# Kernel tuning notes

Hardware: AMD Instinct MI355X
Metric: run time of the kernel (lower is better)

Reference implementation:

```python
import jax, jax.numpy as jnp
import numpy as np
import math

B, S, E, H = 2, 2048, 512, 8
D = E // H
EPS = 1e-6
MAXN = 1.0 - 1e-5  # stay strictly inside the Poincare ball


def _norm(x):
    return jnp.sqrt(jnp.clip(jnp.sum(x * x, axis=-1, keepdims=True), 1e-12))


def expmap0(u):
    n = _norm(u)
    return jnp.tanh(n) * u / n


def logmap0(x):
    n = _norm(x)
    return jnp.arctanh(jnp.clip(n, None, MAXN)) * x / n


def hlinear(x, W, b):
    # HLinear: Mobius matvec == expmap0(W @ logmap0(x)), tangent bias
    return expmap0(logmap0(x) @ W.T + b)


def _lbeta(a, b):
    return math.lgamma(a) + math.lgamma(b) - math.lgamma(a + b)


def setup_inputs() -> dict:
    key = jax.random.key(0)
    ks = jax.random.split(key, 6)

    def pt(k, shape):  # random points on the Poincare ball
        return expmap0(0.2 * jax.random.normal(k, shape, dtype=jnp.float32))

    return {
        "query": pt(ks[0], (B, S, E)),
        "key": pt(ks[1], (B, S, E)),
        "value": pt(ks[2], (B, S, E)),
        "Wq": jax.random.normal(ks[3], (E, E), jnp.float32) / math.sqrt(E),
        "Wk": jax.random.normal(ks[4], (E, E), jnp.float32) / math.sqrt(E),
        "Wv": jax.random.normal(ks[5], (E, E), jnp.float32) / math.sqrt(E),
        "bq": jnp.zeros((E,), jnp.float32),
        "bk": jnp.zeros((E,), jnp.float32),
        "bv": jnp.zeros((E,), jnp.float32),
        "scale_tau": jnp.zeros((1,), jnp.float32),
        "scale_gamma": jnp.zeros((1,), jnp.float32),
    }


def reference(query, key, value, Wq, Wk, Wv, bq, bk, bv, scale_tau, scale_gamma):
    # hyperbolic q/k/v projections, then split heads: [B,H,S,D]
    q = hlinear(query, Wq, bq).reshape(B, S, H, D).transpose(0, 2, 1, 3)
    k = hlinear(key, Wk, bk).reshape(B, S, H, D).transpose(0, 2, 1, 3)
    v = hlinear(value, Wv, bv).reshape(B, S, H, D).transpose(0, 2, 1, 3)

    # pairwise Poincare distance via norms + dot (no [S,S,D] intermediate)
    qn2 = jnp.sum(q * q, -1)                       # [B,H,S]
    kn2 = jnp.sum(k * k, -1)                       # [B,H,S]
    dot = jnp.einsum('bhid,bhjd->bhij', q, k)      # [B,H,S,S]
    sq = jnp.clip(qn2[..., :, None] + kn2[..., None, :] - 2.0 * dot, 0.0)
    denom = jnp.clip((1.0 - qn2)[..., :, None] * (1.0 - kn2)[..., None, :], EPS)
    dist = jnp.arccosh(jnp.clip(1.0 + 2.0 * sq / denom, 1.0 + 1e-7))

    # attention_similarity: -d / tau + gamma, tau = 1/exp(scale_tau)
    sim = -dist * jnp.exp(scale_tau[0]) + scale_gamma[0]

    # causal mask + 'exp' activation (masked_fill(-inf) then exp -> 0)
    mask = jnp.triu(jnp.ones((S, S), bool), 1)
    w = jnp.where(mask, 0.0, jnp.exp(sim))         # [B,H,S,S]

    # gyromidpoint: (1/2) (x) [sum_j w lam_j v_j / sum_j w (lam_j - 1)]
    vn2 = jnp.sum(v * v, -1)
    lam = 2.0 / jnp.clip(1.0 - vn2, EPS)           # [B,H,S]
    num = jnp.einsum('bhij,bhjd->bhid', w, v * lam[..., None])
    den = jnp.einsum('bhij,bhj->bhi', w, lam - 1.0)
    m = num / jnp.clip(den, EPS)[..., None]
    mn = _norm(m)
    mid = jnp.tanh(0.5 * jnp.arctanh(jnp.clip(mn, None, MAXN))) * m / mn

    # beta-concatenation of heads back to embed_dim
    beta_ratio = math.exp(_lbeta(E / 2.0, 0.5) - _lbeta(D / 2.0, 0.5))
    t = logmap0(mid) * beta_ratio                  # [B,H,S,D]
    t = t.transpose(0, 2, 1, 3).reshape(B, S, E)
    return expmap0(t)
```

## Files before the change

### kernel.cpp

```cpp
#include <hip/hip_runtime.h>
#include <cmath>

#define BB 2
#define SS 2048
#define EE 512
#define HH 8
#define DD 64

typedef unsigned short u16t;
typedef __bf16 bf16x8 __attribute__((ext_vector_type(8)));
typedef float f32x4 __attribute__((ext_vector_type(4)));

__device__ __forceinline__ float bf2f(u16t u){
    union{unsigned int i; float f;} c; c.i = ((unsigned int)u)<<16; return c.f;
}
__device__ __forceinline__ u16t f2bf(float x){
    union{float f; unsigned int i;} c; c.f = x;
    return (u16t)((c.i + 0x7fffu + ((c.i>>16)&1u))>>16);
}
__device__ __forceinline__ unsigned cvtpk(float a, float b){
    unsigned r;
    asm("v_cvt_pk_bf16_f32 %0, %1, %2" : "=v"(r) : "v"(a), "v"(b));
    return r;
}
__device__ __forceinline__ float fast_tanh(float x){
    float e = __expf(2.f*x); return 1.f - 2.f/(e+1.f);
}
__device__ __forceinline__ float fast_atanh(float x){
    return 0.5f*__logf((1.f+x)/(1.f-x));
}
__device__ __forceinline__ f32x4 mfma16(bf16x8 a, bf16x8 b, f32x4 c){
    return __builtin_amdgcn_mfma_f32_16x16x32_bf16(a,b,c,0,0,0);
}
__device__ __forceinline__ int offq8(int qi){
    int a = qi >> 3;
    return 4*a*(a+1) + (qi & 7)*(a+1);
}

__global__ __launch_bounds__(256) void k_pre(const float* __restrict__ qp,
                                             const float* __restrict__ kp,
                                             const float* __restrict__ vp,
                                             u16t* __restrict__ Tlog,
                                             const float* __restrict__ Wq,
                                             const float* __restrict__ Wk,
                                             const float* __restrict__ Wv,
                                             u16t* __restrict__ Wb){
    int bx = blockIdx.x;
    if (bx < 3072){
        int gr = bx*4 + (threadIdx.x>>6);
        int t = gr >> 12;
        int row = gr & 4095;
        int lane = threadIdx.x & 63;
        const float* src = (t==0 ? qp : (t==1 ? kp : vp)) + (size_t)row*EE;
        const float4* s4 = (const float4*)(src + lane*8);
        float4 a = s4[0], b = s4[1];
        float x[8] = {a.x,a.y,a.z,a.w,b.x,b.y,b.z,b.w};
        float p = 0.f;
        #pragma unroll
        for (int i=0;i<8;++i) p += x[i]*x[i];
        #pragma unroll
        for (int off=32; off>=1; off>>=1) p += __shfl_xor(p, off, 64);
        float n = sqrtf(fmaxf(p, 1e-12f));
        float f = fast_atanh(fminf(n, 1.0f-1e-5f)) / n;
        u16t yb[8];
        #pragma unroll
        for (int i=0;i<8;++i) yb[i] = f2bf(f*x[i]);
        uint4 o;
        o.x = (unsigned)yb[0] | ((unsigned)yb[1]<<16);
        o.y = (unsigned)yb[2] | ((unsigned)yb[3]<<16);
        o.z = (unsigned)yb[4] | ((unsigned)yb[5]<<16);
        o.w = (unsigned)yb[6] | ((unsigned)yb[7]<<16);
        *(uint4*)(Tlog + ((size_t)(t*4096+row)*EE + lane*8)) = o;
    } else {
        int idx = ((bx-3072)*256 + threadIdx.x)*4;
        int t = idx >> 18;
        int off = idx & 262143;
        const float* W = (t==0 ? Wq : (t==1 ? Wk : Wv));
        float4 a = *(const float4*)(W + off);
        uint2 o;
        o.x = (unsigned)f2bf(a.x) | ((unsigned)f2bf(a.y)<<16);
        o.y = (unsigned)f2bf(a.z) | ((unsigned)f2bf(a.w)<<16);
        *(uint2*)(Wb + idx) = o;
    }
}

__global__ __launch_bounds__(256) void k_proj(const u16t* __restrict__ Tlog,
                                              const u16t* __restrict__ Wb,
                                              const float* __restrict__ bq,
                                              const float* __restrict__ bk,
                                              const float* __restrict__ bv,
                                              u16t* __restrict__ U){
    __shared__ __align__(16) u16t Wl[64][72];
    int bx = blockIdx.x;
    int t = bx >> 9; int rem = bx & 511;
    int m0 = (rem >> 3) << 6; int n0 = (rem & 7) << 6;
    int tid = threadIdx.x; int wv = tid>>6; int lane = tid&63;
    int l15 = lane & 15; int l4 = lane >> 4;
    const u16t* Tt = Tlog + (size_t)t*4096*EE;
    const u16t* Wt = Wb + (size_t)t*EE*EE;
    const float* bias = (t==0 ? bq : (t==1 ? bk : bv));
    f32x4 z = {0.f,0.f,0.f,0.f};
    f32x4 acc[4] = {z,z,z,z};
    int arow = m0 + 16*wv + l15;
    int rr = tid >> 2; int cc = (tid & 3) * 16;
    uint4 w0, w1;
    {
        const uint4* g = (const uint4*)(Wt + (size_t)(n0+rr)*EE + cc);
        w0 = g[0]; w1 = g[1];
    }
    for (int ks=0; ks<8; ++ks){
        int k0 = ks*64;
        *(uint4*)&Wl[rr][cc]   = w0;
        *(uint4*)&Wl[rr][cc+8] = w1;
        __syncthreads();
        if (ks < 7){
            const uint4* g = (const uint4*)(Wt + (size_t)(n0+rr)*EE + k0 + 64 + cc);
            w0 = g[0]; w1 = g[1];
        }
        bf16x8 a0 = *(const bf16x8*)(Tt + (size_t)arow*EE + k0 + l4*8);
        bf16x8 a1 = *(const bf16x8*)(Tt + (size_t)arow*EE + k0 + 32 + l4*8);
        #pragma unroll
        for (int f=0; f<4; ++f){
            bf16x8 b0 = *(const bf16x8*)&Wl[f*16+l15][l4*8];
            bf16x8 b1 = *(const bf16x8*)&Wl[f*16+l15][32+l4*8];
            acc[f] = mfma16(b0, a0, acc[f]);
            acc[f] = mfma16(b1, a1, acc[f]);
        }
        __syncthreads();
    }
    u16t* Ut = U + (size_t)t*4096*EE;
    int mrow = m0 + 16*wv + l15;
    #pragma unroll
    for (int f=0; f<4; ++f){
        float4 b4 = *(const float4*)&bias[n0 + f*16 + l4*4];
        uint2 u2;
        u2.x = cvtpk(acc[f][0]+b4.x, acc[f][1]+b4.y);
        u2.y = cvtpk(acc[f][2]+b4.z, acc[f][3]+b4.w);
        *(uint2*)(Ut + (size_t)mrow*EE + n0 + f*16 + l4*4) = u2;
    }
}

__global__ __launch_bounds__(256) void k_expmap_split(const u16t* __restrict__ U,
        u16t* __restrict__ Q, u16t* __restrict__ K, u16t* __restrict__ VT,
        float* __restrict__ qn2, float* __restrict__ kn2, float* __restrict__ lam1){
    int gr = blockIdx.x*4 + (threadIdx.x>>6);
    int t = gr >> 12;
    int row = gr & 4095;
    int b = row >> 11; int s = row & 2047;
    int lane = threadIdx.x & 63;
    const u16t* u = U + ((size_t)t*4096 + row)*EE;
    uint4 raw = *(const uint4*)(u + lane*8);
    const u16t* rs = (const u16t*)&raw;
    float x[8];
    #pragma unroll
    for (int i=0;i<8;++i) x[i] = bf2f(rs[i]);
    float p = 0.f;
    #pragma unroll
    for (int i=0;i<8;++i) p += x[i]*x[i];
    #pragma unroll
    for (int off=32; off>=1; off>>=1) p += __shfl_xor(p, off, 64);
    float n = sqrtf(fmaxf(p, 1e-12f));
    float f = fast_tanh(n)/n;
    float y[8]; u16t yb[8];
    float hp = 0.f;
    #pragma unroll
    for (int i=0;i<8;++i){
        yb[i] = f2bf(f*x[i]);
        y[i]  = bf2f(yb[i]);
        hp += y[i]*y[i];
    }
    #pragma unroll
    for (int off=1; off<8; off<<=1) hp += __shfl_xor(hp, off, 64);
    hp = fminf(hp, 0.99999988f);
    int h = lane >> 3;
    size_t ih = (size_t)(b*HH + h)*SS + s;
    if (t == 0){
        uint4 o;
        o.x=(unsigned)yb[0]|((unsigned)yb[1]<<16); o.y=(unsigned)yb[2]|((unsigned)yb[3]<<16);
        o.z=(unsigned)yb[4]|((unsigned)yb[5]<<16); o.w=(unsigned)yb[6]|((unsigned)yb[7]<<16);
        *(uint4*)(Q + ih*DD + (lane&7)*8) = o;
        if ((lane&7)==0) qn2[ih] = hp;
    } else if (t == 1){
        uint4 o;
        o.x=(unsigned)yb[0]|((unsigned)yb[1]<<16); o.y=(unsigned)yb[2]|((unsigned)yb[3]<<16);
        o.z=(unsigned)yb[4]|((unsigned)yb[5]<<16); o.w=(unsigned)yb[6]|((unsigned)yb[7]<<16);
        *(uint4*)(K + ih*DD + (lane&7)*8) = o;
        if ((lane&7)==0) kn2[ih] = hp;
    } else {
        float lam = 2.f / fmaxf(1.f - hp, 1e-6f);
        size_t bh = (size_t)(b*HH + h);
        int d0 = (lane&7)*8;
        #pragma unroll
        for (int i=0;i<8;++i)
            VT[(bh*DD + d0 + i)*SS + s] = f2bf(y[i]*lam);
        if ((lane&7)==0) lam1[ih] = lam - 1.f;
    }
}

#define EW_BLOCK(DO_DIAG, FASTW)                                              \
    _Pragma("unroll")                                                         \
    for (int f=0; f<4; ++f){                                                  \
        float4 kn24 = *(const float4*)&kn2s[f*16 + l4*4];                     \
        float4 akf4 = *(const float4*)&akfs[f*16 + l4*4];                     \
        float4 l14  = *(const float4*)&l1s [f*16 + l4*4];                     \
        float wv4[4];                                                         \
        _Pragma("unroll")                                                     \
        for (int r=0; r<4; ++r){                                              \
            float sq  = fmaxf(fmaf(-2.f, c[f][r], qv + ((const float*)&kn24)[r]), 0.f); \
            float co  = fminf(aq2 * ((const float*)&akf4)[r], 2e6f);          \
            float rho = sq * co;                                              \
            float tt  = fmaf(rho, rho, rho + rho);                            \
            float zz  = 1.f + rho + __builtin_amdgcn_sqrtf(tt);               \
            float w;                                                          \
            if (FASTW){ w = __builtin_amdgcn_rcpf(zz); }                      \
            else { float L = __builtin_amdgcn_logf(zz);                       \
                   w = __builtin_amdgcn_exp2f(fmaf(-tauexp, L, gm2)); }       \
            if (DO_DIAG && (kv0 + f*16 + l4*4 + r) > qrow) w = 0.f;           \
            dn = fmaf(w, ((const float*)&l14)[r], dn);                        \
            wv4[r] = w;                                                       \
        }                                                                     \
        uint2 u2; u2.x = cvtpk(wv4[0], wv4[1]); u2.y = cvtpk(wv4[2], wv4[3]); \
        *(uint2*)&Wt[16*wv + l15][f*16 + l4*4] = u2;                          \
    }

__global__ __launch_bounds__(256,5) void k_attn(const u16t* __restrict__ Q,
        const u16t* __restrict__ K, const u16t* __restrict__ VT,
        const float* __restrict__ qn2, const float* __restrict__ kn2,
        const float* __restrict__ lam1, const float* __restrict__ taup,
        const float* __restrict__ gammap,
        float* __restrict__ pnum, float* __restrict__ pden){
    __shared__ __align__(16) u16t Kt[64][72];
    __shared__ __align__(16) u16t Vt[64][72];
    __shared__ __align__(16) u16t Wt[64][72];
    __shared__ float kn2s[64], akfs[64], l1s[64];
    int bx = blockIdx.x;
    int bh = bx & 15;
    int u = bx >> 4;
    int v = 79 - u;
    int qi = 31;
    while (offq8(qi) > v) --qi;
    int c0 = v - offq8(qi);
    int jt0 = c0 << 3;
    int jt1 = min(jt0 + 8, qi + 1);
    int s0 = qi << 6;
    int tid = threadIdx.x; int wv = tid>>6; int lane = tid&63;
    int l15 = lane & 15; int l4 = lane >> 4;
    float tauexp = __expf(taup[0]);
    float gm2 = gammap[0] * 1.44269504088896340736f;
    bool fastw = (tauexp == 1.0f) && (gm2 == 0.0f);
    size_t base = (size_t)bh * SS;
    int qrow = s0 + 16*wv + l15;
    bf16x8 aQ0 = *(const bf16x8*)(Q + (base + qrow)*DD + l4*8);
    bf16x8 aQ1 = *(const bf16x8*)(Q + (base + qrow)*DD + 32 + l4*8);
    float qv  = qn2[base + qrow];
    float aq2 = 2.f * __builtin_amdgcn_rcpf(fmaxf(1.f - qv, 1e-6f));
    f32x4 z4 = {0.f,0.f,0.f,0.f};
    f32x4 num[4] = {z4,z4,z4,z4};
    float dn = 0.f;
    int rr = tid >> 2; int cc = (tid & 3) << 4;
    uint4 pka0, pka1, pva0, pva1; float pkn = 0.f, pl1 = 0.f;
    {
        int kv0 = jt0 << 6;
        const uint4* gk = (const uint4*)(K + (base + kv0 + rr)*DD + cc);
        pka0 = gk[0]; pka1 = gk[1];
        const uint4* gv = (const uint4*)(VT + ((size_t)bh*DD + rr)*SS + kv0 + cc);
        pva0 = gv[0]; pva1 = gv[1];
        if (tid < 64){ pkn = kn2[base+kv0+tid]; pl1 = lam1[base+kv0+tid]; }
    }
    for (int jt=jt0; jt<jt1; ++jt){
        *(uint4*)&Kt[rr][cc]   = pka0;
        *(uint4*)&Kt[rr][cc+8] = pka1;
        *(uint4*)&Vt[rr][cc]   = pva0;
        *(uint4*)&Vt[rr][cc+8] = pva1;
        if (tid < 64){
            kn2s[tid] = pkn;
            l1s[tid]  = pl1;
            akfs[tid] = __builtin_amdgcn_rcpf(fmaxf(1.f - pkn, 1e-6f));
        }
        __syncthreads();
        if (jt+1 < jt1){
            int kv0n = (jt+1) << 6;
            const uint4* gk = (const uint4*)(K + (base + kv0n + rr)*DD + cc);
            pka0 = gk[0]; pka1 = gk[1];
            const uint4* gv = (const uint4*)(VT + ((size_t)bh*DD + rr)*SS + kv0n + cc);
            pva0 = gv[0]; pva1 = gv[1];
            if (tid < 64){ pkn = kn2[base+kv0n+tid]; pl1 = lam1[base+kv0n+tid]; }
        }
        int kv0 = jt << 6;
        f32x4 c[4] = {z4,z4,z4,z4};
        #pragma unroll
        for (int f=0; f<4; ++f){
            bf16x8 kb0 = *(const bf16x8*)&Kt[f*16+l15][l4*8];
            bf16x8 kb1 = *(const bf16x8*)&Kt[f*16+l15][32+l4*8];
            c[f] = mfma16(kb0, aQ0, c[f]);
            c[f] = mfma16(kb1, aQ1, c[f]);
        }
        if (jt == qi){
            if (fastw) { EW_BLOCK(true, true) } else { EW_BLOCK(true, false) }
        } else {
            if (fastw) { EW_BLOCK(false, true) } else { EW_BLOCK(false, false) }
        }
        bf16x8 pw0 = *(const bf16x8*)&Wt[16*wv + l15][l4*8];
        bf16x8 pw1 = *(const bf16x8*)&Wt[16*wv + l15][32 + l4*8];
        #pragma unroll
        for (int f=0; f<4; ++f){
            bf16x8 vb0 = *(const bf16x8*)&Vt[f*16+l15][l4*8];
            bf16x8 vb1 = *(const bf16x8*)&Vt[f*16+l15][32+l4*8];
            num[f] = mfma16(vb0, pw0, num[f]);
            num[f] = mfma16(vb1, pw1, num[f]);
        }
        __syncthreads();
    }
    dn += __shfl_xor(dn, 16, 64);
    dn += __shfl_xor(dn, 32, 64);
    size_t pidx = (size_t)bh*80 + offq8(qi) + c0;
    float* pn = pnum + pidx*4096;
    #pragma unroll
    for (int f=0; f<4; ++f)
        *(f32x4*)&pn[(16*wv + l15)*64 + f*16 + l4*4] = num[f];
    if (l4 == 0) pden[pidx*64 + 16*wv + l15] = dn;
}

__global__ __launch_bounds__(256) void k_post(const float* __restrict__ pnum,
        const float* __restrict__ pden, float* __restrict__ out, float beta){
    int bx = blockIdx.x;
    int b = bx >> 7; int stile = bx & 127;
    int tid = threadIdx.x;
    int row = tid >> 4; int h = (tid >> 1) & 7; int half = tid & 1;
    int s = stile*16 + row;
    int qi = s >> 6; int rowin = s & 63;
    int nch = (qi >> 3) + 1;
    size_t pb = (size_t)(b*HH + h)*80 + offq8(qi);
    float mv[32];
    #pragma unroll
    for (int i=0;i<32;++i) mv[i] = 0.f;
    float den = 0.f;
    for (int cc=0; cc<nch; ++cc){
        const float* pn = pnum + (pb+cc)*4096 + rowin*64 + half*32;
        #pragma unroll
        for (int i=0;i<8;++i){
            float4 v = *(const float4*)(pn + i*4);
            mv[i*4+0]+=v.x; mv[i*4+1]+=v.y; mv[i*4+2]+=v.z; mv[i*4+3]+=v.w;
        }
        den += pden[(pb+cc)*64 + rowin];
    }
    float invd = 1.f / fmaxf(den, 1e-6f);
    float mn2h = 0.f;
    #pragma unroll
    for (int i=0;i<32;++i){ mv[i] *= invd; mn2h += mv[i]*mv[i]; }
    float mn2 = mn2h + __shfl_xor(mn2h, 1, 64);
    float mn = sqrtf(fmaxf(mn2, 1e-12f));
    float g = beta * 0.5f * fast_atanh(fminf(mn, 1.0f-1e-5f)) / mn;
    float tn = g*g*mn2;
    tn += __shfl_xor(tn, 2, 64);
    tn += __shfl_xor(tn, 4, 64);
    tn += __shfl_xor(tn, 8, 64);
    float en = sqrtf(fmaxf(tn, 1e-12f));
    float f = fast_tanh(en)/en;
    float gf = g * f;
    float* dst = out + ((size_t)(b*SS + s))*EE + h*DD + half*32;
    #pragma unroll
    for (int i=0;i<8;++i){
        float4 v = {gf*mv[i*4+0], gf*mv[i*4+1], gf*mv[i*4+2], gf*mv[i*4+3]};
        *(float4*)(dst + i*4) = v;
    }
}

extern "C" void kernel_launch(void* const* d_in, const int* in_sizes, int n_in,
                              void* d_out, int out_size, void* d_ws, size_t ws_size,
                              hipStream_t stream) {
    const float* q_in  = (const float*)d_in[0];
    const float* k_in  = (const float*)d_in[1];
    const float* v_in  = (const float*)d_in[2];
    const float* Wq    = (const float*)d_in[3];
    const float* Wk    = (const float*)d_in[4];
    const float* Wv    = (const float*)d_in[5];
    const float* bq    = (const float*)d_in[6];
    const float* bk    = (const float*)d_in[7];
    const float* bv    = (const float*)d_in[8];
    const float* tau   = (const float*)d_in[9];
    const float* gamma = (const float*)d_in[10];
    float* out = (float*)d_out;

    char* ws = (char*)d_ws;
    u16t*  Tlog = (u16t*)(ws + 0);
    u16t*  Wb   = (u16t*)(ws + 12582912);
    u16t*  Ub   = (u16t*)(ws + 14155776);
    u16t*  Qb   = (u16t*)(ws + 26738688);
    u16t*  Kb   = (u16t*)(ws + 30932992);
    u16t*  VTb  = (u16t*)(ws + 35127296);
    float* qn2  = (float*)(ws + 39321600);
    float* kn2  = (float*)(ws + 39452672);
    float* lam1 = (float*)(ws + 39583744);
    float* pnum = (float*)(ws + 39714816);
    float* pden = (float*)(ws + 60686336);

    double lb1 = std::lgamma(256.0) + std::lgamma(0.5) - std::lgamma(256.5);
    double lb2 = std::lgamma(32.0)  + std::lgamma(0.5) - std::lgamma(32.5);
    float beta = (float)std::exp(lb1 - lb2);

    k_pre<<<3840, 256, 0, stream>>>(q_in, k_in, v_in, Tlog, Wq, Wk, Wv, Wb);
    k_proj<<<1536, 256, 0, stream>>>(Tlog, Wb, bq, bk, bv, Ub);
    k_expmap_split<<<3072, 256, 0, stream>>>(Ub, Qb, Kb, VTb, qn2, kn2, lam1);
    k_attn<<<1280, 256, 0, stream>>>(Qb, Kb, VTb, qn2, kn2, lam1, tau, gamma,
                                     pnum, pden);
    k_post<<<256, 256, 0, stream>>>(pnum, pden, out, beta);
}
```

Before: 91.17 us.

## Fuse logmap0 and weight bf16 conversion into projection GEMM

Result: slower. 133.0 us (+45.8%).

```diff
diff --git a/kernel.cpp b/kernel.cpp
--- a/kernel.cpp
+++ b/kernel.cpp
@@ -37,106 +37,88 @@
     return 4*a*(a+1) + (qi & 7)*(a+1);
 }
 
-__global__ __launch_bounds__(256) void k_pre(const float* __restrict__ qp,
-                                             const float* __restrict__ kp,
-                                             const float* __restrict__ vp,
-                                             u16t* __restrict__ Tlog,
-                                             const float* __restrict__ Wq,
-                                             const float* __restrict__ Wk,
-                                             const float* __restrict__ Wv,
-                                             u16t* __restrict__ Wb){
-    int bx = blockIdx.x;
-    if (bx < 3072){
-        int gr = bx*4 + (threadIdx.x>>6);
-        int t = gr >> 12;
-        int row = gr & 4095;
-        int lane = threadIdx.x & 63;
-        const float* src = (t==0 ? qp : (t==1 ? kp : vp)) + (size_t)row*EE;
-        const float4* s4 = (const float4*)(src + lane*8);
-        float4 a = s4[0], b = s4[1];
-        float x[8] = {a.x,a.y,a.z,a.w,b.x,b.y,b.z,b.w};
-        float p = 0.f;
-        #pragma unroll
-        for (int i=0;i<8;++i) p += x[i]*x[i];
-        #pragma unroll
-        for (int off=32; off>=1; off>>=1) p += __shfl_xor(p, off, 64);
-        float n = sqrtf(fmaxf(p, 1e-12f));
-        float f = fast_atanh(fminf(n, 1.0f-1e-5f)) / n;
-        u16t yb[8];
-        #pragma unroll
-        for (int i=0;i<8;++i) yb[i] = f2bf(f*x[i]);
-        uint4 o;
-        o.x = (unsigned)yb[0] | ((unsigned)yb[1]<<16);
-        o.y = (unsigned)yb[2] | ((unsigned)yb[3]<<16);
-        o.z = (unsigned)yb[4] | ((unsigned)yb[5]<<16);
-        o.w = (unsigned)yb[6] | ((unsigned)yb[7]<<16);
-        *(uint4*)(Tlog + ((size_t)(t*4096+row)*EE + lane*8)) = o;
-    } else {
-        int idx = ((bx-3072)*256 + threadIdx.x)*4;
-        int t = idx >> 18;
-        int off = idx & 262143;
-        const float* W = (t==0 ? Wq : (t==1 ? Wk : Wv));
-        float4 a = *(const float4*)(W + off);
-        uint2 o;
-        o.x = (unsigned)f2bf(a.x) | ((unsigned)f2bf(a.y)<<16);
-        o.y = (unsigned)f2bf(a.z) | ((unsigned)f2bf(a.w)<<16);
-        *(uint2*)(Wb + idx) = o;
-    }
-}
-
-__global__ __launch_bounds__(256) void k_proj(const u16t* __restrict__ Tlog,
-                                              const u16t* __restrict__ Wb,
-                                              const float* __restrict__ bq,
-                                              const float* __restrict__ bk,
-                                              const float* __restrict__ bv,
-                                              u16t* __restrict__ U){
+__global__ __launch_bounds__(256) void k_proj(const float* __restrict__ qp,
+        const float* __restrict__ kp, const float* __restrict__ vp,
+        const float* __restrict__ Wq, const float* __restrict__ Wk,
+        const float* __restrict__ Wv,
+        const float* __restrict__ bq, const float* __restrict__ bk,
+        const float* __restrict__ bv,
+        u16t* __restrict__ U){
     __shared__ __align__(16) u16t Wl[64][72];
     int bx = blockIdx.x;
     int t = bx >> 9; int rem = bx & 511;
     int m0 = (rem >> 3) << 6; int n0 = (rem & 7) << 6;
-    int tid = threadIdx.x; int wv = tid>>6; int lane = tid&63;
+    int tid = threadIdx.x; int wvi = tid>>6; int lane = tid&63;
     int l15 = lane & 15; int l4 = lane >> 4;
-    const u16t* Tt = Tlog + (size_t)t*4096*EE;
-    const u16t* Wt = Wb + (size_t)t*EE*EE;
+    const float* X  = (t==0 ? qp : (t==1 ? kp : vp));
+    const float* Wf = (t==0 ? Wq : (t==1 ? Wk : Wv));
     const float* bias = (t==0 ? bq : (t==1 ? bk : bv));
+    int arow = m0 + 16*wvi + l15;
+    const float* xr = X + (size_t)arow*EE;
+    float pn = 0.f;
+    #pragma unroll
+    for (int i=0;i<32;++i){
+        float4 v = *(const float4*)(xr + l4*128 + i*4);
+        pn += v.x*v.x + v.y*v.y + v.z*v.z + v.w*v.w;
+    }
+    pn += __shfl_xor(pn,16,64); pn += __shfl_xor(pn,32,64);
+    float nn = sqrtf(fmaxf(pn, 1e-12f));
+    float sc = fast_atanh(fminf(nn, 1.0f-1e-5f)) / nn;
     f32x4 z = {0.f,0.f,0.f,0.f};
     f32x4 acc[4] = {z,z,z,z};
-    int arow = m0 + 16*wv + l15;
     int rr = tid >> 2; int cc = (tid & 3) * 16;
-    uint4 w0, w1;
-    {
-        const uint4* g = (const uint4*)(Wt + (size_t)(n0+rr)*EE + cc);
-        w0 = g[0]; w1 = g[1];
-    }
+    const float* wrow = Wf + (size_t)(n0+rr)*EE;
+    float4 w0 = *(const float4*)(wrow + cc);
+    float4 w1 = *(const float4*)(wrow + cc + 4);
+    float4 w2 = *(const float4*)(wrow + cc + 8);
+    float4 w3 = *(const float4*)(wrow + cc + 12);
+    float4 a00 = *(const float4*)(xr + l4*8);
+    float4 a01 = *(const float4*)(xr + l4*8 + 4);
+    float4 a10 = *(const float4*)(xr + 32 + l4*8);
+    float4 a11 = *(const float4*)(xr + 32 + l4*8 + 4);
     for (int ks=0; ks<8; ++ks){
         int k0 = ks*64;
-        *(uint4*)&Wl[rr][cc]   = w0;
-        *(uint4*)&Wl[rr][cc+8] = w1;
+        uint4 wa, wb;
+        wa.x = cvtpk(w0.x,w0.y); wa.y = cvtpk(w0.z,w0.w);
+        wa.z = cvtpk(w1.x,w1.y); wa.w = cvtpk(w1.z,w1.w);
+        wb.x = cvtpk(w2.x,w2.y); wb.y = cvtpk(w2.z,w2.w);
+        wb.z = cvtpk(w3.x,w3.y); wb.w = cvtpk(w3.z,w3.w);
+        *(uint4*)&Wl[rr][cc]   = wa;
+        *(uint4*)&Wl[rr][cc+8] = wb;
+        union { uint4 u; bf16x8 v; } ua0, ua1;
+        ua0.u.x = cvtpk(a00.x,a00.y); ua0.u.y = cvtpk(a00.z,a00.w);
+        ua0.u.z = cvtpk(a01.x,a01.y); ua0.u.w = cvtpk(a01.z,a01.w);
+        ua1.u.x = cvtpk(a10.x,a10.y); ua1.u.y = cvtpk(a10.z,a10.w);
+        ua1.u.z = cvtpk(a11.x,a11.y); ua1.u.w = cvtpk(a11.z,a11.w);
         __syncthreads();
         if (ks < 7){
-            const uint4* g = (const uint4*)(Wt + (size_t)(n0+rr)*EE + k0 + 64 + cc);
-            w0 = g[0]; w1 = g[1];
-        }
-        bf16x8 a0 = *(const bf16x8*)(Tt + (size_t)arow*EE + k0 + l4*8);
-        bf16x8 a1 = *(const bf16x8*)(Tt + (size_t)arow*EE + k0 + 32 + l4*8);
+            int kn = k0 + 64;
+            w0 = *(const float4*)(wrow + kn + cc);
+            w1 = *(const float4*)(wrow + kn + cc + 4);
+            w2 = *(const float4*)(wrow + kn + cc + 8);
+            w3 = *(const float4*)(wrow + kn + cc + 12);
+            a00 = *(const float4*)(xr + kn + l4*8);
+            a01 = *(const float4*)(xr + kn + l4*8 + 4);
+            a10 = *(const float4*)(xr + kn + 32 + l4*8);
+            a11 = *(const float4*)(xr + kn + 32 + l4*8 + 4);
+        }
         #pragma unroll
         for (int f=0; f<4; ++f){
             bf16x8 b0 = *(const bf16x8*)&Wl[f*16+l15][l4*8];
             bf16x8 b1 = *(const bf16x8*)&Wl[f*16+l15][32+l4*8];
-            acc[f] = mfma16(b0, a0, acc[f]);
-            acc[f] = mfma16(b1, a1, acc[f]);
+            acc[f] = mfma16(b0, ua0.v, acc[f]);
+            acc[f] = mfma16(b1, ua1.v, acc[f]);
         }
         __syncthreads();
     }
     u16t* Ut = U + (size_t)t*4096*EE;
-    int mrow = m0 + 16*wv + l15;
     #pragma unroll
     for (int f=0; f<4; ++f){
         float4 b4 = *(const float4*)&bias[n0 + f*16 + l4*4];
         uint2 u2;
-        u2.x = cvtpk(acc[f][0]+b4.x, acc[f][1]+b4.y);
-        u2.y = cvtpk(acc[f][2]+b4.z, acc[f][3]+b4.w);
-        *(uint2*)(Ut + (size_t)mrow*EE + n0 + f*16 + l4*4) = u2;
+        u2.x = cvtpk(fmaf(sc,acc[f][0],b4.x), fmaf(sc,acc[f][1],b4.y));
+        u2.y = cvtpk(fmaf(sc,acc[f][2],b4.z), fmaf(sc,acc[f][3],b4.w));
+        *(uint2*)(Ut + (size_t)arow*EE + n0 + f*16 + l4*4) = u2;
     }
 }
 
@@ -383,24 +365,22 @@
     float* out = (float*)d_out;
 
     char* ws = (char*)d_ws;
-    u16t*  Tlog = (u16t*)(ws + 0);
-    u16t*  Wb   = (u16t*)(ws + 12582912);
-    u16t*  Ub   = (u16t*)(ws + 14155776);
-    u16t*  Qb   = (u16t*)(ws + 26738688);
-    u16t*  Kb   = (u16t*)(ws + 30932992);
-    u16t*  VTb  = (u16t*)(ws + 35127296);
-    float* qn2  = (float*)(ws + 39321600);
-    float* kn2  = (float*)(ws + 39452672);
-    float* lam1 = (float*)(ws + 39583744);
-    float* pnum = (float*)(ws + 39714816);
-    float* pden = (float*)(ws + 60686336);
+    u16t*  Ub   = (u16t*)(ws + 0);
+    u16t*  Qb   = (u16t*)(ws + 12582912);
+    u16t*  Kb   = (u16t*)(ws + 16777216);
+    u16t*  VTb  = (u16t*)(ws + 20971520);
+    float* qn2  = (float*)(ws + 25165824);
+    float* kn2  = (float*)(ws + 25296896);
+    float* lam1 = (float*)(ws + 25427968);
+    float* pnum = (float*)(ws + 25559040);
+    float* pden = (float*)(ws + 46530560);
 
     double lb1 = std::lgamma(256.0) + std::lgamma(0.5) - std::lgamma(256.5);
     double lb2 = std::lgamma(32.0)  + std::lgamma(0.5) - std::lgamma(32.5);
     float beta = (float)std::exp(lb1 - lb2);
 
-    k_pre<<<3840, 256, 0, stream>>>(q_in, k_in, v_in, Tlog, Wq, Wk, Wv, Wb);
-    k_proj<<<1536, 256, 0, stream>>>(Tlog, Wb, bq, bk, bv, Ub);
+    k_proj<<<1536, 256, 0, stream>>>(q_in, k_in, v_in, Wq, Wk, Wv,
+                                     bq, bk, bv, Ub);
     k_expmap_split<<<3072, 256, 0, stream>>>(Ub, Qb, Kb, VTb, qn2, kn2, lam1);
     k_attn<<<1280, 256, 0, stream>>>(Qb, Kb, VTb, qn2, kn2, lam1, tau, gamma,
                                      pnum, pden);
```

## Double-buffer K/V tiles, drop trailing barrier, use 16-tile KV chunks

Applied to the files above, without the earlier changes.

New measurement: 92.66 us. About the same (+1.6%).

```diff
diff --git a/kernel.cpp b/kernel.cpp
--- a/kernel.cpp
+++ b/kernel.cpp
@@ -32,9 +32,8 @@
 __device__ __forceinline__ f32x4 mfma16(bf16x8 a, bf16x8 b, f32x4 c){
     return __builtin_amdgcn_mfma_f32_16x16x32_bf16(a,b,c,0,0,0);
 }
-__device__ __forceinline__ int offq8(int qi){
-    int a = qi >> 3;
-    return 4*a*(a+1) + (qi & 7)*(a+1);
+__device__ __forceinline__ int offq16(int qi){
+    return (qi < 16) ? qi : (2*qi - 16);
 }
 
 __global__ __launch_bounds__(256) void k_pre(const float* __restrict__ qp,
@@ -200,9 +199,9 @@
 #define EW_BLOCK(DO_DIAG, FASTW)                                              \
     _Pragma("unroll")                                                         \
     for (int f=0; f<4; ++f){                                                  \
-        float4 kn24 = *(const float4*)&kn2s[f*16 + l4*4];                     \
-        float4 akf4 = *(const float4*)&akfs[f*16 + l4*4];                     \
-        float4 l14  = *(const float4*)&l1s [f*16 + l4*4];                     \
+        float4 kn24 = *(const float4*)&kn2s[cur][f*16 + l4*4];                \
+        float4 akf4 = *(const float4*)&akfs[cur][f*16 + l4*4];                \
+        float4 l14  = *(const float4*)&l1s [cur][f*16 + l4*4];                \
         float wv4[4];                                                         \
         _Pragma("unroll")                                                     \
         for (int r=0; r<4; ++r){                                              \
@@ -223,25 +222,25 @@
         *(uint2*)&Wt[16*wv + l15][f*16 + l4*4] = u2;                          \
     }
 
-__global__ __launch_bounds__(256,5) void k_attn(const u16t* __restrict__ Q,
+__global__ __launch_bounds__(256,3) void k_attn(const u16t* __restrict__ Q,
         const u16t* __restrict__ K, const u16t* __restrict__ VT,
         const float* __restrict__ qn2, const float* __restrict__ kn2,
         const float* __restrict__ lam1, const float* __restrict__ taup,
         const float* __restrict__ gammap,
         float* __restrict__ pnum, float* __restrict__ pden){
-    __shared__ __align__(16) u16t Kt[64][72];
-    __shared__ __align__(16) u16t Vt[64][72];
+    __shared__ __align__(16) u16t Kt[2][64][72];
+    __shared__ __align__(16) u16t Vt[2][64][72];
     __shared__ __align__(16) u16t Wt[64][72];
-    __shared__ float kn2s[64], akfs[64], l1s[64];
+    __shared__ float kn2s[2][64], akfs[2][64], l1s[2][64];
     int bx = blockIdx.x;
     int bh = bx & 15;
     int u = bx >> 4;
-    int v = 79 - u;
-    int qi = 31;
-    while (offq8(qi) > v) --qi;
-    int c0 = v - offq8(qi);
-    int jt0 = c0 << 3;
-    int jt1 = min(jt0 + 8, qi + 1);
+    int v = 47 - u;
+    int qi, c0;
+    if (v < 16){ qi = v; c0 = 0; }
+    else { qi = (v + 16) >> 1; c0 = (v + 16) & 1; }
+    int jt0 = c0 << 4;
+    int jt1 = min(jt0 + 16, qi + 1);
     int s0 = qi << 6;
     int tid = threadIdx.x; int wv = tid>>6; int lane = tid&63;
     int l15 = lane & 15; int l4 = lane >> 4;
@@ -267,15 +266,16 @@
         pva0 = gv[0]; pva1 = gv[1];
         if (tid < 64){ pkn = kn2[base+kv0+tid]; pl1 = lam1[base+kv0+tid]; }
     }
+    int cur = 0;
     for (int jt=jt0; jt<jt1; ++jt){
-        *(uint4*)&Kt[rr][cc]   = pka0;
-        *(uint4*)&Kt[rr][cc+8] = pka1;
-        *(uint4*)&Vt[rr][cc]   = pva0;
-        *(uint4*)&Vt[rr][cc+8] = pva1;
+        *(uint4*)&Kt[cur][rr][cc]   = pka0;
+        *(uint4*)&Kt[cur][rr][cc+8] = pka1;
+        *(uint4*)&Vt[cur][rr][cc]   = pva0;
+        *(uint4*)&Vt[cur][rr][cc+8] = pva1;
         if (tid < 64){
-            kn2s[tid] = pkn;
-            l1s[tid]  = pl1;
-            akfs[tid] = __builtin_amdgcn_rcpf(fmaxf(1.f - pkn, 1e-6f));
+            kn2s[cur][tid] = pkn;
+            l1s[cur][tid]  = pl1;
+            akfs[cur][tid] = __builtin_amdgcn_rcpf(fmaxf(1.f - pkn, 1e-6f));
         }
         __syncthreads();
         if (jt+1 < jt1){
@@ -290,8 +290,8 @@
         f32x4 c[4] = {z4,z4,z4,z4};
         #pragma unroll
         for (int f=0; f<4; ++f){
-            bf16x8 kb0 = *(const bf16x8*)&Kt[f*16+l15][l4*8];
-            bf16x8 kb1 = *(const bf16x8*)&Kt[f*16+l15][32+l4*8];
+            bf16x8 kb0 = *(const bf16x8*)&Kt[cur][f*16+l15][l4*8];
+            bf16x8 kb1 = *(const bf16x8*)&Kt[cur][f*16+l15][32+l4*8];
             c[f] = mfma16(kb0, aQ0, c[f]);
             c[f] = mfma16(kb1, aQ1, c[f]);
         }
@@ -304,16 +304,16 @@
         bf16x8 pw1 = *(const bf16x8*)&Wt[16*wv + l15][32 + l4*8];
         #pragma unroll
         for (int f=0; f<4; ++f){
-            bf16x8 vb0 = *(const bf16x8*)&Vt[f*16+l15][l4*8];
-            bf16x8 vb1 = *(const bf16x8*)&Vt[f*16+l15][32+l4*8];
+            bf16x8 vb0 = *(const bf16x8*)&Vt[cur][f*16+l15][l4*8];
+            bf16x8 vb1 = *(const bf16x8*)&Vt[cur][f*16+l15][32+l4*8];
             num[f] = mfma16(vb0, pw0, num[f]);
             num[f] = mfma16(vb1, pw1, num[f]);
         }
-        __syncthreads();
+        cur ^= 1;
     }
     dn += __shfl_xor(dn, 16, 64);
     dn += __shfl_xor(dn, 32, 64);
-    size_t pidx = (size_t)bh*80 + offq8(qi) + c0;
+    size_t pidx = (size_t)bh*48 + offq16(qi) + c0;
     float* pn = pnum + pidx*4096;
     #pragma unroll
     for (int f=0; f<4; ++f)
@@ -329,8 +329,8 @@
     int row = tid >> 4; int h = (tid >> 1) & 7; int half = tid & 1;
     int s = stile*16 + row;
     int qi = s >> 6; int rowin = s & 63;
-    int nch = (qi >> 3) + 1;
-    size_t pb = (size_t)(b*HH + h)*80 + offq8(qi);
+    int nch = (qi >> 4) + 1;
+    size_t pb = (size_t)(b*HH + h)*48 + offq16(qi);
     float mv[32];
     #pragma unroll
     for (int i=0;i<32;++i) mv[i] = 0.f;
@@ -393,7 +393,7 @@
     float* kn2  = (float*)(ws + 39452672);
     float* lam1 = (float*)(ws + 39583744);
     float* pnum = (float*)(ws + 39714816);
-    float* pden = (float*)(ws + 60686336);
+    float* pden = (float*)(ws + 52297728);
 
     double lb1 = std::lgamma(256.0) + std::lgamma(0.5) - std::lgamma(256.5);
     double lb2 = std::lgamma(32.0)  + std::lgamma(0.5) - std::lgamma(32.5);
@@ -402,7 +402,7 @@
     k_pre<<<3840, 256, 0, stream>>>(q_in, k_in, v_in, Tlog, Wq, Wk, Wv, Wb);
     k_proj<<<1536, 256, 0, stream>>>(Tlog, Wb, bq, bk, bv, Ub);
     k_expmap_split<<<3072, 256, 0, stream>>>(Ub, Qb, Kb, VTb, qn2, kn2, lam1);
-    k_attn<<<1280, 256, 0, stream>>>(Qb, Kb, VTb, qn2, kn2, lam1, tau, gamma,
-                                     pnum, pden);
+    k_attn<<<768, 256, 0, stream>>>(Qb, Kb, VTb, qn2, kn2, lam1, tau, gamma,
+                                    pnum, pden);
     k_post<<<256, 256, 0, stream>>>(pnum, pden, out, beta);
 }
```
